# Performance work log

Hardware: AMD Instinct MI355X
Metric: run time of the kernel (lower is better)

Reference implementation:

```python
import jax, jax.numpy as jnp
import numpy as np

D_MODEL = 4096
NUM_EXPERTS = 64
TOP_K = 2


def setup_inputs() -> dict:
    key = jax.random.key(0)
    kx, kw, kb = jax.random.split(key, 3)
    x = jax.random.normal(kx, (4, 4096, D_MODEL), dtype=jnp.float32)
    # nn.Linear(d_model, num_experts): weight [E, D], bias [E]
    bound = 1.0 / np.sqrt(D_MODEL)
    W = jax.random.uniform(kw, (NUM_EXPERTS, D_MODEL), jnp.float32, -bound, bound)
    b = jax.random.uniform(kb, (NUM_EXPERTS,), jnp.float32, -bound, bound)
    return {"x": x, "W": W, "b": b}


def reference(x, W, b):
    # gate: logits over experts  [B, S, E]
    logits = jnp.einsum("bsd,ed->bse", x, W) + b
    # top-k experts per token
    top_w, top_i = jax.lax.top_k(logits, TOP_K)  # [B, S, K]
    # softmax over the selected k logits
    top_w = jax.nn.softmax(top_w, axis=-1)
    return top_w, top_i
```

## Files before the change

kernel.cpp:

```cpp
#include <hip/hip_runtime.h>
#include <math.h>

#define D_MODEL 4096
#define NE 64
#define TPB 64
#define NSTEPS 64
#define BUFB 32768
#define WS_SHORTS (256 * 2 * 64 * 8)

typedef __attribute__((ext_vector_type(8))) short short8;
typedef __attribute__((ext_vector_type(16))) float f32x16;

__device__ __forceinline__ void gl_lds(const void* g, void* l) {
    __builtin_amdgcn_global_load_lds(
        (const __attribute__((address_space(1))) unsigned*)g,
        (__attribute__((address_space(3))) unsigned*)l, 16, 0, 0);
}

__device__ __forceinline__ void split8(const float4& a, const float4& c,
                                       short8& h8, short8& l8) {
    union { short8 s; unsigned u[4]; } H, L;
    float vv[8] = {a.x, a.y, a.z, a.w, c.x, c.y, c.z, c.w};
#pragma unroll
    for (int p = 0; p < 4; p++) {
        const float v0 = vv[2*p], v1 = vv[2*p+1];
        const unsigned u0 = __float_as_uint(v0), u1 = __float_as_uint(v1);
        const unsigned r0 = u0 + 0x7fffu + ((u0 >> 16) & 1u);
        const unsigned r1 = u1 + 0x7fffu + ((u1 >> 16) & 1u);
        const float lo0 = v0 - __uint_as_float(r0 & 0xffff0000u);
        const float lo1 = v1 - __uint_as_float(r1 & 0xffff0000u);
        H.u[p] = __builtin_amdgcn_perm(r1, r0, 0x07060302u);
        L.u[p] = __builtin_amdgcn_perm(__float_as_uint(lo1),
                                       __float_as_uint(lo0), 0x07060302u);
    }
    h8 = H.s; l8 = L.s;
}

__global__ void wsplit_kernel(const float* __restrict__ W, short* __restrict__ wsp) {
    const int ck = blockIdx.x, t = threadIdx.x;
    const int nt = t >> 6, l = t & 63;
    const float* wp = W + (size_t)(nt * 32 + (l & 31)) * D_MODEL + ck * 16 + (l >> 5) * 8;
    float4 a = *(const float4*)wp, c = *(const float4*)(wp + 4);
    union { short8 s; unsigned u[4]; } H, L;
    float vv[8] = {a.x, a.y, a.z, a.w, c.x, c.y, c.z, c.w};
#pragma unroll
    for (int p = 0; p < 4; p++) {
        const float v0 = vv[2*p], v1 = vv[2*p+1];
        const unsigned u0 = __float_as_uint(v0), u1 = __float_as_uint(v1);
        const unsigned r0 = u0 + 0x7fffu + ((u0 >> 16) & 1u);
        const unsigned r1 = u1 + 0x7fffu + ((u1 >> 16) & 1u);
        const float lo0 = v0 - __uint_as_float(r0 & 0xffff0000u);
        const float lo1 = v1 - __uint_as_float(r1 & 0xffff0000u);
        const unsigned q0 = __float_as_uint(lo0) + 0x7fffu + ((__float_as_uint(lo0) >> 16) & 1u);
        const unsigned q1 = __float_as_uint(lo1) + 0x7fffu + ((__float_as_uint(lo1) >> 16) & 1u);
        H.u[p] = __builtin_amdgcn_perm(r1, r0, 0x07060302u);
        L.u[p] = __builtin_amdgcn_perm(q1, q0, 0x07060302u);
    }
    const size_t off = ((size_t)(ck * 2 + nt) * 64 + l) * 8;
    *(short8*)(wsp + off)             = H.s;
    *(short8*)(wsp + WS_SHORTS + off) = L.s;
}

#define MF(A_, B_, n_) acc[n_] = __builtin_amdgcn_mfma_f32_32x32x16_bf16( \
                             A_, B_, acc[n_], 0, 0, 0)

__global__ __launch_bounds__(512) void router_pipe(
    const float* __restrict__ x, const short* __restrict__ wsp,
    const float* __restrict__ b, float* __restrict__ out, int T)
{
    __shared__ char smem[4 * BUFB];

    const int tid  = threadIdx.x;
    const int wv   = tid >> 6, lane = tid & 63;
    const int mt   = wv & 1;
    const int kq   = wv >> 1;
    const int tok0 = blockIdx.x * TPB;

    const int tokA = tid >> 4, clA = tid & 15;
    const int tokB = 32 + tokA;
    const float* gx1 = x + (size_t)(tok0 + tokA) * D_MODEL + ((clA ^ (tokA & 15)) * 4);
    const float* gx2 = x + (size_t)(tok0 + tokB) * D_MODEL + ((clA ^ (tokB & 15)) * 4);
    const char* whi = (const char*)wsp + (size_t)tid * 16;
    const char* wlo = (const char*)(wsp + WS_SHORTS) + (size_t)tid * 16;

#define STAGE(sc_, bi_) do {                                                  \
        char* db_ = smem + (bi_) * BUFB + wv * 1024;                          \
        gl_lds(gx1 + (size_t)(sc_) * 64, db_);                                \
        gl_lds(gx2 + (size_t)(sc_) * 64, db_ + 8192);                         \
        gl_lds(whi + (size_t)(sc_) * 8192, db_ + 16384);                      \
        gl_lds(wlo + (size_t)(sc_) * 8192, db_ + 24576);                      \
    } while (0)

    f32x16 acc[2];
#pragma unroll
    for (int e = 0; e < 16; e++) { acc[0][e] = 0.f; acc[1][e] = 0.f; }

    const int row = mt * 32 + (lane & 31);
    const int c0  = kq * 4 + (lane >> 5) * 2;
    const int xo1 = row * 256 + ((c0     ^ (row & 15)) * 16);
    const int xo2 = row * 256 + (((c0+1) ^ (row & 15)) * 16);
    const int wo0 = 16384 + ((kq * 2 + 0) * 64 + lane) * 16;
    const int wo1 = 16384 + ((kq * 2 + 1) * 64 + lane) * 16;

    STAGE(0, 0);
    STAGE(1, 1);

    for (int s = 0; s < NSTEPS; ++s) {
        const int sc = (s + 2 < NSTEPS) ? s + 2 : NSTEPS - 1;
        STAGE(sc, (s + 2) & 3);
        asm volatile("s_waitcnt vmcnt(8)" ::: "memory");
        __builtin_amdgcn_s_barrier();
        __builtin_amdgcn_sched_barrier(0);
        const char* buf = smem + (s & 3) * BUFB;
        float4 xa = *(const float4*)(buf + xo1);
        float4 xb = *(const float4*)(buf + xo2);
        short8 b0h = *(const short8*)(buf + wo0);
        short8 b1h = *(const short8*)(buf + wo1);
        short8 b0l = *(const short8*)(buf + wo0 + 8192);
        short8 b1l = *(const short8*)(buf + wo1 + 8192);
        short8 Ah, Al;
        split8(xa, xb, Ah, Al);
        MF(Ah, b0h, 0); MF(Ah, b0l, 0); MF(Al, b0h, 0); MF(Al, b0l, 0);
        MF(Ah, b1h, 1); MF(Ah, b1l, 1); MF(Al, b1h, 1); MF(Al, b1l, 1);
    }
#undef STAGE

    asm volatile("s_waitcnt vmcnt(0)" ::: "memory");
    __builtin_amdgcn_s_barrier();
    __builtin_amdgcn_sched_barrier(0);

    float* red = (float*)smem;
    auto store_slab = [&](int slab) {
        float* sl = red + ((size_t)slab * 64 + lane) * 32;
#pragma unroll
        for (int q = 0; q < 8; q++) {
            const int nt = q >> 2, rg = (q & 3) * 4;
            *(float4*)(sl + ((q + lane) & 7) * 4) =
                make_float4(acc[nt][rg], acc[nt][rg+1], acc[nt][rg+2], acc[nt][rg+3]);
        }
    };
    auto add_slab = [&](int slab) {
        const float* sl = red + ((size_t)slab * 64 + lane) * 32;
#pragma unroll
        for (int q = 0; q < 8; q++) {
            const int nt = q >> 2, rg = (q & 3) * 4;
            float4 v = *(const float4*)(sl + ((q + lane) & 7) * 4);
            acc[nt][rg] += v.x; acc[nt][rg+1] += v.y;
            acc[nt][rg+2] += v.z; acc[nt][rg+3] += v.w;
        }
    };
    if (kq >= 2) store_slab(mt * 2 + (kq - 2));
    __syncthreads();
    if (kq < 2) add_slab(mt * 2 + kq);
    __syncthreads();
    if (kq == 1) store_slab(mt);
    __syncthreads();
    if (kq == 0) add_slab(mt);
    __syncthreads();

    float* lg = (float*)(smem + 49152);
    if (kq == 0) {
        const int h = lane >> 5, c31 = lane & 31;
        const float bb0 = b[c31], bb1 = b[32 + c31];
#pragma unroll
        for (int nt = 0; nt < 2; nt++) {
#pragma unroll
            for (int e = 0; e < 16; e++) {
                const int r2 = (e & 3) + 8 * (e >> 2) + 4 * h;
                lg[(mt * 32 + r2) * 68 + nt * 32 + c31] = acc[nt][e] + (nt ? bb1 : bb0);
            }
        }
    }
    __syncthreads();

    if (tid < TPB) {
        const float4* rowp = (const float4*)(lg + tid * 68);
        float v0 = -INFINITY, v1 = -INFINITY;
        int i0 = 0, i1 = 0;
#pragma unroll
        for (int q = 0; q < 16; q++) {
            float4 v4 = rowp[q];
            float vs[4] = {v4.x, v4.y, v4.z, v4.w};
#pragma unroll
            for (int j = 0; j < 4; j++) {
                const int e = q * 4 + j;
                const float v = vs[j];
                if (v > v0)      { v1 = v0; i1 = i0; v0 = v; i0 = e; }
                else if (v > v1) { v1 = v;  i1 = e; }
            }
        }
        const float e1 = expf(v1 - v0);
        const float w0 = 1.f / (1.f + e1);
        const int tok = tok0 + tid;
        out[tok * 2 + 0] = w0;
        out[tok * 2 + 1] = e1 * w0;
        float* oi = out + (size_t)T * 2;
        oi[tok * 2 + 0] = (float)i0;
        oi[tok * 2 + 1] = (float)i1;
    }
}

__global__ __launch_bounds__(512, 4) void router_fb(
    const float* __restrict__ x, const float* __restrict__ W,
    const float* __restrict__ b, float* __restrict__ out, int T)
{
    __shared__ short smem[16384];
    const int tid = threadIdx.x;
    const int wv = tid >> 6, lane = tid & 63;
    const int tok0 = blockIdx.x * 32;
    const int row = lane & 31, kh = lane >> 5;
    const float* gx = x + (size_t)(tok0 + row) * D_MODEL + wv * 512 + kh * 8;
    f32x16 acc[2];
#pragma unroll
    for (int e = 0; e < 16; e++) { acc[0][e] = 0.f; acc[1][e] = 0.f; }
    for (int s = 0; s < 32; s++) {
        const float* g = gx + (size_t)s * 16;
        float4 xa = *(const float4*)g, xb = *(const float4*)(g + 4);
        const int k0 = wv * 512 + s * 16 + kh * 8;
        const float* w0 = W + (size_t)row * D_MODEL + k0;
        const float* w1 = W + (size_t)(32 + row) * D_MODEL + k0;
        short8 Ah, Al, B0h, B0l, B1h, B1l;
        split8(xa, xb, Ah, Al);
        split8(*(const float4*)w0, *(const float4*)(w0 + 4), B0h, B0l);
        split8(*(const float4*)w1, *(const float4*)(w1 + 4), B1h, B1l);
        MF(Ah, B0h, 0); MF(Ah, B0l, 0); MF(Al, B0h, 0); MF(Al, B0l, 0);
        MF(Ah, B1h, 1); MF(Ah, B1l, 1); MF(Al, B1h, 1); MF(Al, B1l, 1);
    }
    float* red = (float*)smem;
    auto store_slab = [&](int slab) {
        float* sl = red + ((size_t)slab * 64 + lane) * 32;
#pragma unroll
        for (int q = 0; q < 8; q++) {
            const int nt = q >> 2, rg = (q & 3) * 4;
            *(float4*)(sl + ((q + lane) & 7) * 4) =
                make_float4(acc[nt][rg], acc[nt][rg+1], acc[nt][rg+2], acc[nt][rg+3]);
        }
    };
    auto add_slab = [&](int slab) {
        const float* sl = red + ((size_t)slab * 64 + lane) * 32;
#pragma unroll
        for (int q = 0; q < 8; q++) {
            const int nt = q >> 2, rg = (q & 3) * 4;
            float4 v = *(const float4*)(sl + ((q + lane) & 7) * 4);
            acc[nt][rg] += v.x; acc[nt][rg+1] += v.y;
            acc[nt][rg+2] += v.z; acc[nt][rg+3] += v.w;
        }
    };
    __syncthreads();
    if (wv >= 4) store_slab(wv - 4);
    __syncthreads();
    if (wv < 4) add_slab(wv);
    __syncthreads();
    if (wv == 2 || wv == 3) store_slab(wv - 2);
    __syncthreads();
    if (wv < 2) add_slab(wv);
    __syncthreads();
    if (wv == 1) store_slab(0);
    __syncthreads();
    if (wv == 0) add_slab(0);
    __syncthreads();
    float* lg = (float*)smem;
    if (wv == 0) {
        const int h = lane >> 5, c31 = lane & 31;
        const float bb0 = b[c31], bb1 = b[32 + c31];
#pragma unroll
        for (int nt = 0; nt < 2; nt++)
#pragma unroll
            for (int e = 0; e < 16; e++) {
                const int r2 = (e & 3) + 8 * (e >> 2) + 4 * h;
                lg[r2 * 68 + nt * 32 + c31] = acc[nt][e] + (nt ? bb1 : bb0);
            }
    }
    __syncthreads();
    if (tid < 32) {
        const float4* rowp = (const float4*)(lg + tid * 68);
        float v0 = -INFINITY, v1 = -INFINITY;
        int i0 = 0, i1 = 0;
#pragma unroll
        for (int q = 0; q < 16; q++) {
            float4 v4 = rowp[q];
            float vs[4] = {v4.x, v4.y, v4.z, v4.w};
#pragma unroll
            for (int j = 0; j < 4; j++) {
                const float v = vs[j];
                if (v > v0)      { v1 = v0; i1 = i0; v0 = v; i0 = q*4+j; }
                else if (v > v1) { v1 = v;  i1 = q*4+j; }
            }
        }
        const float e1 = expf(v1 - v0);
        const float w0 = 1.f / (1.f + e1);
        const int tok = tok0 + tid;
        out[tok * 2 + 0] = w0;
        out[tok * 2 + 1] = e1 * w0;
        float* oi = out + (size_t)T * 2;
        oi[tok * 2 + 0] = (float)i0;
        oi[tok * 2 + 1] = (float)i1;
    }
}

extern "C" void kernel_launch(void* const* d_in, const int* in_sizes, int n_in,
                              void* d_out, int out_size, void* d_ws, size_t ws_size,
                              hipStream_t stream) {
    const float* x = (const float*)d_in[0];
    const float* W = (const float*)d_in[1];
    const float* b = (const float*)d_in[2];
    float* out = (float*)d_out;
    short* wsp = (short*)d_ws;
    const int T = in_sizes[0] / D_MODEL;

    const bool pre = (ws_size >= (size_t)(2 * WS_SHORTS) * sizeof(short));
    if (pre) {
        hipLaunchKernelGGL(wsplit_kernel, dim3(256), dim3(128), 0, stream, W, wsp);
        hipLaunchKernelGGL(router_pipe, dim3(T / TPB), dim3(512), 0, stream,
                           x, wsp, b, out, T);
    } else {
        hipLaunchKernelGGL(router_fb, dim3(T / 32), dim3(512), 0, stream,
                           x, W, b, out, T);
    }
}
```

Measured before the change: 69.73 us.

## Load router weights directly to registers and shrink LDS staging for occupancy

The split bf16 weight tiles are now read by each wave straight from global memory into registers, software-pipelined one step ahead with two register sets. Only the x tiles are still staged through LDS with global_load_lds. This halves the LDS footprint (128 KB to 64 KB), and launch bounds now request 2 blocks per CU so more waves can hide latency. The trade-offs are higher register pressure from the extra weight registers under the tighter launch bound, and more intricate vmcnt accounting in the unrolled pipeline.

New measurement: 67.20 us. -3.6%, faster.

```diff
diff --git a/kernel.cpp b/kernel.cpp
--- a/kernel.cpp
+++ b/kernel.cpp
@@ -5,7 +5,8 @@
 #define NE 64
 #define TPB 64
 #define NSTEPS 64
-#define BUFB 32768
+#define XBUF 16384
+#define NXBUF 4
 #define WS_SHORTS (256 * 2 * 64 * 8)
 
 typedef __attribute__((ext_vector_type(8))) short short8;
@@ -64,11 +65,11 @@
 #define MF(A_, B_, n_) acc[n_] = __builtin_amdgcn_mfma_f32_32x32x16_bf16( \
                              A_, B_, acc[n_], 0, 0, 0)
 
-__global__ __launch_bounds__(512) void router_pipe(
+__global__ __launch_bounds__(512, 2) void router_pipe(
     const float* __restrict__ x, const short* __restrict__ wsp,
     const float* __restrict__ b, float* __restrict__ out, int T)
 {
-    __shared__ char smem[4 * BUFB];
+    __shared__ char smem[NXBUF * XBUF];
 
     const int tid  = threadIdx.x;
     const int wv   = tid >> 6, lane = tid & 63;
@@ -80,16 +81,26 @@
     const int tokB = 32 + tokA;
     const float* gx1 = x + (size_t)(tok0 + tokA) * D_MODEL + ((clA ^ (tokA & 15)) * 4);
     const float* gx2 = x + (size_t)(tok0 + tokB) * D_MODEL + ((clA ^ (tokB & 15)) * 4);
-    const char* whi = (const char*)wsp + (size_t)tid * 16;
-    const char* wlo = (const char*)(wsp + WS_SHORTS) + (size_t)tid * 16;
-
-#define STAGE(sc_, bi_) do {                                                  \
-        char* db_ = smem + (bi_) * BUFB + wv * 1024;                          \
-        gl_lds(gx1 + (size_t)(sc_) * 64, db_);                                \
-        gl_lds(gx2 + (size_t)(sc_) * 64, db_ + 8192);                         \
-        gl_lds(whi + (size_t)(sc_) * 8192, db_ + 16384);                      \
-        gl_lds(wlo + (size_t)(sc_) * 8192, db_ + 24576);                      \
-    } while (0)
+
+#define STAGEX(s_, bi_) do { char* db_ = smem + (bi_) * XBUF + wv * 1024;      \
+        gl_lds(gx1 + (size_t)(s_) * 64, db_);                                  \
+        gl_lds(gx2 + (size_t)(s_) * 64, db_ + 8192);                           \
+        __builtin_amdgcn_sched_barrier(0); } while (0)
+
+#define LDW(s_, W0_, W1_, W2_, W3_) do {                                       \
+        const size_t ck_ = (size_t)(s_) * 4 + kq;                              \
+        const size_t o0_ = ((ck_ * 2 + 0) * 64 + lane) * 8;                    \
+        const size_t o1_ = ((ck_ * 2 + 1) * 64 + lane) * 8;                    \
+        W0_ = *(const short8*)(wsp + o0_);                                     \
+        W1_ = *(const short8*)(wsp + o1_);                                     \
+        W2_ = *(const short8*)(wsp + WS_SHORTS + o0_);                         \
+        W3_ = *(const short8*)(wsp + WS_SHORTS + o1_);                         \
+        __builtin_amdgcn_sched_barrier(0); } while (0)
+
+#define FENCE(n_) do { asm volatile("s_waitcnt vmcnt(" #n_ ")" ::: "memory");  \
+        __builtin_amdgcn_sched_barrier(0); } while (0)
+#define BAR do { __builtin_amdgcn_s_barrier();                                 \
+        __builtin_amdgcn_sched_barrier(0); } while (0)
 
     f32x16 acc[2];
 #pragma unroll
@@ -97,37 +108,40 @@
 
     const int row = mt * 32 + (lane & 31);
     const int c0  = kq * 4 + (lane >> 5) * 2;
-    const int xo1 = row * 256 + ((c0     ^ (row & 15)) * 16);
-    const int xo2 = row * 256 + (((c0+1) ^ (row & 15)) * 16);
-    const int wo0 = 16384 + ((kq * 2 + 0) * 64 + lane) * 16;
-    const int wo1 = 16384 + ((kq * 2 + 1) * 64 + lane) * 16;
-
-    STAGE(0, 0);
-    STAGE(1, 1);
-
-    for (int s = 0; s < NSTEPS; ++s) {
-        const int sc = (s + 2 < NSTEPS) ? s + 2 : NSTEPS - 1;
-        STAGE(sc, (s + 2) & 3);
-        asm volatile("s_waitcnt vmcnt(8)" ::: "memory");
-        __builtin_amdgcn_s_barrier();
-        __builtin_amdgcn_sched_barrier(0);
-        const char* buf = smem + (s & 3) * BUFB;
-        float4 xa = *(const float4*)(buf + xo1);
-        float4 xb = *(const float4*)(buf + xo2);
-        short8 b0h = *(const short8*)(buf + wo0);
-        short8 b1h = *(const short8*)(buf + wo1);
-        short8 b0l = *(const short8*)(buf + wo0 + 8192);
-        short8 b1l = *(const short8*)(buf + wo1 + 8192);
-        short8 Ah, Al;
-        split8(xa, xb, Ah, Al);
-        MF(Ah, b0h, 0); MF(Ah, b0l, 0); MF(Al, b0h, 0); MF(Al, b0l, 0);
-        MF(Ah, b1h, 1); MF(Ah, b1l, 1); MF(Al, b1h, 1); MF(Al, b1l, 1);
-    }
-#undef STAGE
-
-    asm volatile("s_waitcnt vmcnt(0)" ::: "memory");
-    __builtin_amdgcn_s_barrier();
-    __builtin_amdgcn_sched_barrier(0);
+    const int xo1 = row * 256 + ((c0       ^ (row & 15)) * 16);
+    const int xo2 = row * 256 + (((c0 + 1) ^ (row & 15)) * 16);
+
+#define COMPUTE(bi_, W0_, W1_, W2_, W3_) do {                                  \
+        const char* buf_ = smem + (bi_) * XBUF;                                \
+        float4 xa_ = *(const float4*)(buf_ + xo1);                             \
+        float4 xb_ = *(const float4*)(buf_ + xo2);                             \
+        short8 Ah_, Al_;                                                       \
+        split8(xa_, xb_, Ah_, Al_);                                            \
+        MF(Ah_, W0_, 0); MF(Ah_, W2_, 0); MF(Al_, W0_, 0); MF(Al_, W2_, 0);    \
+        MF(Ah_, W1_, 1); MF(Ah_, W3_, 1); MF(Al_, W1_, 1); MF(Al_, W3_, 1); } while (0)
+
+    short8 Wa0, Wa1, Wa2, Wa3, Wb0, Wb1, Wb2, Wb3;
+
+    STAGEX(0, 0); STAGEX(1, 1);
+    LDW(0, Wa0, Wa1, Wa2, Wa3);
+
+    for (int t = 0; t < NSTEPS - 2; t += 2) {
+        LDW(t + 1, Wb0, Wb1, Wb2, Wb3);
+        STAGEX(t + 2, (t + 2) & 3);
+        FENCE(8); BAR;
+        COMPUTE(t & 3, Wa0, Wa1, Wa2, Wa3);
+        LDW(t + 2, Wa0, Wa1, Wa2, Wa3);
+        STAGEX(t + 3, (t + 3) & 3);
+        FENCE(8); BAR;
+        COMPUTE((t + 1) & 3, Wb0, Wb1, Wb2, Wb3);
+    }
+    LDW(NSTEPS - 1, Wb0, Wb1, Wb2, Wb3);
+    FENCE(6); BAR;
+    COMPUTE((NSTEPS - 2) & 3, Wa0, Wa1, Wa2, Wa3);
+    FENCE(0); BAR;
+    COMPUTE((NSTEPS - 1) & 3, Wb0, Wb1, Wb2, Wb3);
+
+    __syncthreads();
 
     float* red = (float*)smem;
     auto store_slab = [&](int slab) {
@@ -158,7 +172,7 @@
     if (kq == 0) add_slab(mt);
     __syncthreads();
 
-    float* lg = (float*)(smem + 49152);
+    float* lg = (float*)(smem + 32768);
     if (kq == 0) {
         const int h = lane >> 5, c31 = lane & 31;
         const float bb0 = b[c31], bb1 = b[32 + c31];
```
